# Performance work log

Hardware: AMD Instinct MI355X
Metric: run time of the kernel (lower is better)

Reference implementation:

```python
import jax, jax.numpy as jnp
import numpy as np

B, S, H = 2, 2048, 1024
NH = 16
HD = H // NH


def setup_inputs() -> dict:
    key = jax.random.key(0)
    ks = jax.random.split(key, 9)
    std = 1.0 / np.sqrt(H)
    inp = {"x": jax.random.normal(ks[0], (B, S, H), dtype=jnp.float32)}
    names = ["Wq", "Wk", "Wv", "Wo"]
    for i, n in enumerate(names):
        inp[n] = jax.random.uniform(ks[1 + i], (H, H), dtype=jnp.float32, minval=-std, maxval=std)
        inp["b" + n[1:]] = jax.random.uniform(ks[5 + i], (H,), dtype=jnp.float32, minval=-std, maxval=std)
    return inp


def reference(x, Wq, Wk, Wv, Wo, bq, bk, bv, bo):
    scale = HD ** -0.5
    # projections: torch Linear is x @ W.T + b
    def proj(W, b):
        y = jnp.einsum('bsh,oh->bso', x, W) + b
        return y.reshape(B, S, NH, HD).transpose(0, 2, 1, 3)  # [B, NH, S, HD]
    Q = proj(Wq, bq)
    K = proj(Wk, bk)
    V = proj(Wv, bv)
    scores = jnp.einsum('bhqd,bhkd->bhqk', Q, K) * scale  # [B, NH, S, S]
    attn = jax.nn.softmax(scores, axis=-1)
    ctx = jnp.einsum('bhqk,bhkd->bhqd', attn, V)
    ctx = ctx.transpose(0, 2, 1, 3).reshape(B, S, H)
    out = jnp.einsum('bsh,oh->bso', ctx, Wo) + bo
    avg_attention = attn.mean(axis=1).mean(axis=1)  # [B, S] (mean over heads, then query dim)
    return out, avg_attention
```

## Files before the change

kernel.cpp:

```cpp
#include <hip/hip_runtime.h>
#include <hip/hip_bf16.h>

#define B_  2
#define S_  2048
#define H_  1024
#define NH_ 16
#define HD_ 64
#define NTOK (B_*S_)

typedef __attribute__((ext_vector_type(8))) short bf16x8;
typedef __attribute__((ext_vector_type(4))) float f32x4;

#define SC2 0.18033688011112042f

static __device__ __forceinline__ ushort f2bf(float f) {
    __hip_bfloat16 h = __float2bfloat16(f);
    return *reinterpret_cast<ushort*>(&h);
}
static __device__ __forceinline__ uint cvt_pk_bf16(float lo, float hi) {
    uint r;
    asm("v_cvt_pk_bf16_f32 %0, %1, %2" : "=v"(r) : "v"(lo), "v"(hi));
    return r;
}

static __device__ __forceinline__ void gload_lds16(const void* g, void* l) {
    __builtin_amdgcn_global_load_lds(
        (const __attribute__((address_space(1))) void*)g,
        (__attribute__((address_space(3))) void*)l,
        16, 0, 0);
}

__global__ __launch_bounds__(256) void f32_to_bf16(
    const float* __restrict__ s, ushort* __restrict__ d, int n8)
{
    const int i = blockIdx.x * 256 + threadIdx.x;
    if (i >= n8) return;
    const float4 a = reinterpret_cast<const float4*>(s)[2*i + 0];
    const float4 b = reinterpret_cast<const float4*>(s)[2*i + 1];
    ushort u[8];
    u[0] = f2bf(a.x); u[1] = f2bf(a.y); u[2] = f2bf(a.z); u[3] = f2bf(a.w);
    u[4] = f2bf(b.x); u[5] = f2bf(b.y); u[6] = f2bf(b.z); u[7] = f2bf(b.w);
    reinterpret_cast<uint4*>(d)[i] = *reinterpret_cast<uint4*>(u);
}

struct Cvt4 { const float* s[4]; ushort* d[4]; };
__global__ __launch_bounds__(256) void w_to_bf16(Cvt4 a, int n8)
{
    const int z = blockIdx.y;
    const int i = blockIdx.x * 256 + threadIdx.x;
    if (i >= n8) return;
    const float* s = a.s[z];
    const float4 va = reinterpret_cast<const float4*>(s)[2*i + 0];
    const float4 vb = reinterpret_cast<const float4*>(s)[2*i + 1];
    ushort u[8];
    u[0] = f2bf(va.x); u[1] = f2bf(va.y); u[2] = f2bf(va.z); u[3] = f2bf(va.w);
    u[4] = f2bf(vb.x); u[5] = f2bf(vb.y); u[6] = f2bf(vb.z); u[7] = f2bf(vb.w);
    reinterpret_cast<uint4*>(a.d[z])[i] = *reinterpret_cast<uint4*>(u);
}

__global__ __launch_bounds__(256) void transpose_v(
    const ushort* __restrict__ Vb, ushort* __restrict__ Vt)
{
    __shared__ ushort T[64][72];
    const int t  = threadIdx.x;
    const int b  = blockIdx.z;
    const int h  = blockIdx.y;
    const int s0 = blockIdx.x * 64;
    const int r  = t >> 2;
    const int c0 = (t & 3) * 16;

    const ushort* src = Vb + (size_t)(b*S_ + s0 + r)*H_ + h*HD_ + c0;
    *reinterpret_cast<uint4*>(&T[r][c0])     = *reinterpret_cast<const uint4*>(src);
    *reinterpret_cast<uint4*>(&T[r][c0 + 8]) = *reinterpret_cast<const uint4*>(src + 8);
    __syncthreads();

    const int d = r;
    ushort tmp[16];
#pragma unroll
    for (int k = 0; k < 16; ++k) tmp[k] = T[c0 + k][d];
    ushort* dst = Vt + ((size_t)((b*NH_ + h)*HD_ + d))*S_ + s0 + c0;
    *reinterpret_cast<uint4*>(dst)     = *reinterpret_cast<uint4*>(&tmp[0]);
    *reinterpret_cast<uint4*>(dst + 8) = *reinterpret_cast<uint4*>(&tmp[8]);
}

struct GemmArgs {
    const ushort* W[3];
    const float*  bias[3];
    void*         Y[3];
    float         scale[3];
};

template<int MREP, bool BF16OUT>
__global__ __launch_bounds__(256) void gemm_mfma_bt(
    const ushort* __restrict__ A, GemmArgs args, int M, int N, int K)
{
    constexpr int BM = MREP * 32;
    __shared__ __align__(16) ushort As[BM * 64];
    __shared__ __align__(16) ushort Bs[128 * 64];

    const int z = blockIdx.z;
    const ushort* __restrict__ W   = args.W[z];
    const float*  __restrict__ bia = args.bias[z];
    const float sc = args.scale[z];

    const int t  = threadIdx.x;
    const int w  = t >> 6;
    const int l  = t & 63;
    const int lq = l >> 4;
    const int ln = l & 15;
    const int wr = w >> 1;
    const int wc = w & 1;
    const int m0 = blockIdx.x * BM;
    const int n0 = blockIdx.y * 128;
    const int srow = l >> 3;
    const int scol = (l & 7) * 8;

    f32x4 acc[MREP][4];
#pragma unroll
    for (int m = 0; m < MREP; ++m)
#pragma unroll
        for (int n = 0; n < 4; ++n) acc[m][n] = f32x4{0.f, 0.f, 0.f, 0.f};

    for (int k0 = 0; k0 < K; k0 += 64) {
        __syncthreads();
#pragma unroll
        for (int i = 0; i < BM/32; ++i) {
            const int rb = i*32 + w*8;
            gload_lds16(A + (size_t)(m0 + rb + srow)*K + k0 + scol, &As[rb*64]);
        }
#pragma unroll
        for (int i = 0; i < 4; ++i) {
            const int rb = i*32 + w*8;
            gload_lds16(W + (size_t)(n0 + rb + srow)*K + k0 + scol, &Bs[rb*64]);
        }
        __syncthreads();
#pragma unroll
        for (int ks = 0; ks < 2; ++ks) {
            bf16x8 bfr[4];
#pragma unroll
            for (int n = 0; n < 4; ++n)
                bfr[n] = *reinterpret_cast<const bf16x8*>(&Bs[(wc*64 + n*16 + ln)*64 + ks*32 + lq*8]);
#pragma unroll
            for (int m = 0; m < MREP; ++m) {
                const bf16x8 afr = *reinterpret_cast<const bf16x8*>(&As[(wr*MREP*16 + m*16 + ln)*64 + ks*32 + lq*8]);
#pragma unroll
                for (int n = 0; n < 4; ++n)
                    acc[m][n] = __builtin_amdgcn_mfma_f32_16x16x32_bf16(afr, bfr[n], acc[m][n], 0, 0, 0);
            }
        }
    }

    float bv[4];
#pragma unroll
    for (int n = 0; n < 4; ++n) bv[n] = bia[n0 + wc*64 + n*16 + ln];

#pragma unroll
    for (int m = 0; m < MREP; ++m) {
#pragma unroll
        for (int r = 0; r < 4; ++r) {
            const size_t row = (size_t)(m0 + wr*MREP*16 + m*16 + lq*4 + r);
#pragma unroll
            for (int n = 0; n < 4; ++n) {
                const int col = n0 + wc*64 + n*16 + ln;
                const float val = (acc[m][n][r] + bv[n]) * sc;
                if constexpr (BF16OUT)
                    ((ushort*)args.Y[z])[row*N + col] = f2bf(val);
                else
                    ((float*)args.Y[z])[row*N + col] = val;
            }
        }
    }
}

__global__ __launch_bounds__(256) void attn_pv(
    const ushort* __restrict__ Qb, const ushort* __restrict__ Kb,
    const ushort* __restrict__ Vtg, ushort* __restrict__ ctx,
    float* __restrict__ il2_g)
{
    __shared__ __align__(16) ushort Ks0[64*64];
    __shared__ __align__(16) ushort Ks1[64*64];
    __shared__ __align__(16) ushort Vs0[64*64];
    __shared__ __align__(16) ushort Vs1[64*64];
    __shared__ __align__(16) ushort Ps[4][16*64];

    const int t  = threadIdx.x;
    const int w  = t >> 6;
    const int l  = t & 63;
    const int lq = l >> 4;
    const int ln = l & 15;
    const int b  = blockIdx.z;
    const int h  = blockIdx.y;
    const int q0 = blockIdx.x * 64;
    const int ln7 = ln & 7;

    bf16x8 qf[2];
    {
        const ushort* qrow = Qb + ((size_t)(b*S_ + q0 + w*16 + ln))*H_ + h*HD_ + lq*8;
        qf[0] = *reinterpret_cast<const bf16x8*>(qrow);
        qf[1] = *reinterpret_cast<const bf16x8*>(qrow + 32);
    }

    bf16x8 onesb;
#pragma unroll
    for (int j = 0; j < 8; ++j) onesb[j] = (short)0x3F80;

    size_t koff[2], voff[2];
    int    dsto[2];
#pragma unroll
    for (int i = 0; i < 2; ++i) {
        const int chunk = i*256 + t;
        const int row   = chunk >> 3;
        const int c8    = (chunk & 7) ^ (row & 7);
        koff[i] = (size_t)(b*S_ + row)*H_ + h*HD_ + c8*8;
        voff[i] = ((size_t)((b*NH_ + h)*HD_ + row))*S_ + c8*8;
        dsto[i] = chunk*8;
    }

    f32x4 lsacc = f32x4{0.f, 0.f, 0.f, 0.f};
    f32x4 oacc[4];
#pragma unroll
    for (int nt = 0; nt < 4; ++nt) oacc[nt] = f32x4{0.f, 0.f, 0.f, 0.f};

    auto tile_body = [&](const ushort* __restrict__ ksb, const ushort* __restrict__ vsb,
                         int pre_kt, bool do_pre,
                         ushort* __restrict__ kdst, ushort* __restrict__ vdst) {
        if (do_pre) {
#pragma unroll
            for (int i = 0; i < 2; ++i) {
                gload_lds16(Kb + koff[i] + (size_t)pre_kt*H_, &kdst[dsto[i]]);
                gload_lds16(Vtg + voff[i] + pre_kt, &vdst[dsto[i]]);
            }
        }

        f32x4 sacc[4];
#pragma unroll
        for (int nt = 0; nt < 4; ++nt) sacc[nt] = f32x4{0.f, 0.f, 0.f, 0.f};
#pragma unroll
        for (int ks = 0; ks < 2; ++ks) {
            bf16x8 kb[4];
#pragma unroll
            for (int nt = 0; nt < 4; ++nt)
                kb[nt] = *reinterpret_cast<const bf16x8*>(
                    &ksb[(nt*16 + ln)*64 + (((ks*4 + lq) ^ ln7) * 8)]);
#pragma unroll
            for (int nt = 0; nt < 4; ++nt)
                sacc[nt] = __builtin_amdgcn_mfma_f32_16x16x32_bf16(
                    kb[nt], qf[ks], sacc[nt], 0, 0, 0);
        }

#pragma unroll
        for (int nt = 0; nt < 4; ++nt) {
            const float e0 = exp2f(sacc[nt][0]);
            const float e1 = exp2f(sacc[nt][1]);
            const float e2 = exp2f(sacc[nt][2]);
            const float e3 = exp2f(sacc[nt][3]);
            uint2 pk;
            pk.x = cvt_pk_bf16(e0, e1);
            pk.y = cvt_pk_bf16(e2, e3);
            const int wch = (nt*2 + (lq >> 1)) ^ ln7;
            *reinterpret_cast<uint2*>(&Ps[w][ln*64 + wch*8 + (lq & 1)*4]) = pk;
        }

#pragma unroll
        for (int ks = 0; ks < 2; ++ks) {
            const bf16x8 pa = *reinterpret_cast<const bf16x8*>(
                &Ps[w][ln*64 + (((ks*4 + lq) ^ ln7) * 8)]);
            lsacc = __builtin_amdgcn_mfma_f32_16x16x32_bf16(pa, onesb, lsacc, 0, 0, 0);
#pragma unroll
            for (int nt = 0; nt < 4; ++nt) {
                const bf16x8 vb8 = *reinterpret_cast<const bf16x8*>(
                    &vsb[(nt*16 + ln)*64 + (((ks*4 + lq) ^ ln7) * 8)]);
                oacc[nt] = __builtin_amdgcn_mfma_f32_16x16x32_bf16(
                    pa, vb8, oacc[nt], 0, 0, 0);
            }
        }

        __syncthreads();
    };

#pragma unroll
    for (int i = 0; i < 2; ++i) {
        gload_lds16(Kb + koff[i], &Ks0[dsto[i]]);
        gload_lds16(Vtg + voff[i], &Vs0[dsto[i]]);
    }
    __syncthreads();

    for (int kt = 0; kt < S_; kt += 128) {
        tile_body(Ks0, Vs0, kt + 64, true, Ks1, Vs1);
        tile_body(Ks1, Vs1, kt + 128, kt + 128 < S_, Ks0, Vs0);
    }

    float ivr[4];
#pragma unroll
    for (int r = 0; r < 4; ++r) ivr[r] = 1.f / lsacc[r];

    if (ln == 0) {
        float4 o;
        o.x = -__log2f(lsacc[0]);
        o.y = -__log2f(lsacc[1]);
        o.z = -__log2f(lsacc[2]);
        o.w = -__log2f(lsacc[3]);
        *reinterpret_cast<float4*>(
            il2_g + (size_t)(b*NH_ + h)*S_ + q0 + w*16 + lq*4) = o;
    }

    ushort* crow = ctx + ((size_t)(b*S_ + q0 + w*16 + lq*4))*H_ + h*HD_ + ln;
#pragma unroll
    for (int r = 0; r < 4; ++r)
#pragma unroll
        for (int nt = 0; nt < 4; ++nt)
            crow[(size_t)r*H_ + nt*16] = f2bf(oacc[nt][r] * ivr[r]);
}

__global__ __launch_bounds__(256) void attn_colsum(
    const ushort* __restrict__ Qb, const ushort* __restrict__ Kb,
    const float* __restrict__ il2_g, float* __restrict__ colsum)
{
    __shared__ __align__(16) ushort KsT[64*64];
    __shared__ __align__(16) ushort Qs0[64*64];
    __shared__ __align__(16) ushort Qs1[64*64];
    __shared__ __align__(16) float  iv[S_];

    const int t  = threadIdx.x;
    const int w  = t >> 6;
    const int l  = t & 63;
    const int lq = l >> 4;
    const int ln = l & 15;
    const int b  = blockIdx.z;
    const int h  = blockIdx.y;
    const int k0 = blockIdx.x * 64;
    const int bh = b*NH_ + h;
    const int ln7 = ln & 7;

    int crow_[2], cc8[2], dsto[2];
#pragma unroll
    for (int i = 0; i < 2; ++i) {
        const int chunk = i*256 + t;
        crow_[i] = chunk >> 3;
        cc8[i]   = (chunk & 7) ^ (crow_[i] & 7);
        dsto[i]  = chunk*8;
    }

#pragma unroll
    for (int i = 0; i < 2; ++i) {
        gload_lds16(Kb + (size_t)(b*S_ + k0 + crow_[i])*H_ + h*HD_ + cc8[i]*8, &KsT[dsto[i]]);
        gload_lds16(il2_g + (size_t)bh*S_ + (i*256 + t)*4, &iv[(i*256 + t)*4]);
        gload_lds16(Qb + (size_t)(b*S_ + crow_[i])*H_ + h*HD_ + cc8[i]*8, &Qs0[dsto[i]]);
    }
    __syncthreads();

    bf16x8 kf[2];
#pragma unroll
    for (int ks = 0; ks < 2; ++ks)
        kf[ks] = *reinterpret_cast<const bf16x8*>(
            &KsT[(w*16 + ln)*64 + (((ks*4 + lq) ^ ln7) * 8)]);

    float cs4[4] = {0.f, 0.f, 0.f, 0.f};

    auto tile_body = [&](const ushort* __restrict__ qsb,
                         int pre_qt, bool do_pre, ushort* __restrict__ qdst) {
        if (do_pre) {
#pragma unroll
            for (int i = 0; i < 2; ++i)
                gload_lds16(Qb + (size_t)(b*S_ + pre_qt + crow_[i])*H_ + h*HD_ + cc8[i]*8,
                            &qdst[dsto[i]]);
        }
#pragma unroll
        for (int c = 0; c < 4; ++c) {
            f32x4 sacc = f32x4{0.f, 0.f, 0.f, 0.f};
#pragma unroll
            for (int ks = 0; ks < 2; ++ks) {
                const bf16x8 af = *reinterpret_cast<const bf16x8*>(
                    &qsb[(c*16 + ln)*64 + (((ks*4 + lq) ^ ln7) * 8)]);
                sacc = __builtin_amdgcn_mfma_f32_16x16x32_bf16(af, kf[ks], sacc, 0, 0, 0);
            }
            const f32x4 iv4 = *reinterpret_cast<const f32x4*>(&iv[(c*16 + lq*4) + 0]);
            (void)iv4;
        }
        __syncthreads();
    };
    (void)tile_body;

    int qt = 0;
    for (; qt < S_; qt += 128) {
#pragma unroll
        for (int i = 0; i < 2; ++i)
            gload_lds16(Qb + (size_t)(b*S_ + qt + 64 + crow_[i])*H_ + h*HD_ + cc8[i]*8,
                        &Qs1[dsto[i]]);
#pragma unroll
        for (int c = 0; c < 4; ++c) {
            f32x4 sacc = f32x4{0.f, 0.f, 0.f, 0.f};
#pragma unroll
            for (int ks = 0; ks < 2; ++ks) {
                const bf16x8 af = *reinterpret_cast<const bf16x8*>(
                    &Qs0[(c*16 + ln)*64 + (((ks*4 + lq) ^ ln7) * 8)]);
                sacc = __builtin_amdgcn_mfma_f32_16x16x32_bf16(af, kf[ks], sacc, 0, 0, 0);
            }
            const f32x4 iv4 = *reinterpret_cast<const f32x4*>(&iv[qt + c*16 + lq*4]);
#pragma unroll
            for (int r = 0; r < 4; ++r)
                cs4[r] += exp2f(sacc[r] + iv4[r]);
        }
        __syncthreads();

        if (qt + 128 < S_) {
#pragma unroll
            for (int i = 0; i < 2; ++i)
                gload_lds16(Qb + (size_t)(b*S_ + qt + 128 + crow_[i])*H_ + h*HD_ + cc8[i]*8,
                            &Qs0[dsto[i]]);
        }
#pragma unroll
        for (int c = 0; c < 4; ++c) {
            f32x4 sacc = f32x4{0.f, 0.f, 0.f, 0.f};
#pragma unroll
            for (int ks = 0; ks < 2; ++ks) {
                const bf16x8 af = *reinterpret_cast<const bf16x8*>(
                    &Qs1[(c*16 + ln)*64 + (((ks*4 + lq) ^ ln7) * 8)]);
                sacc = __builtin_amdgcn_mfma_f32_16x16x32_bf16(af, kf[ks], sacc, 0, 0, 0);
            }
            const f32x4 iv4 = *reinterpret_cast<const f32x4*>(&iv[qt + 64 + c*16 + lq*4]);
#pragma unroll
            for (int r = 0; r < 4; ++r)
                cs4[r] += exp2f(sacc[r] + iv4[r]);
        }
        __syncthreads();
    }

    float cs = (cs4[0] + cs4[1]) + (cs4[2] + cs4[3]);
    cs += __shfl_xor(cs, 16);
    cs += __shfl_xor(cs, 32);
    if (l < 16)
        atomicAdd(&colsum[(size_t)b*S_ + k0 + w*16 + l], cs);
}

__global__ void zero_f32(float* p, int n)
{
    const int i = blockIdx.x * 256 + threadIdx.x;
    if (i < n) p[i] = 0.f;
}

__global__ void avg_write(const float* __restrict__ colsum, float* __restrict__ out, float inv)
{
    const int i = blockIdx.x * 256 + threadIdx.x;
    if (i < NTOK) out[i] = colsum[i] * inv;
}

extern "C" void kernel_launch(void* const* d_in, const int* in_sizes, int n_in,
                              void* d_out, int out_size, void* d_ws, size_t ws_size,
                              hipStream_t stream)
{
    const float* x  = (const float*)d_in[0];
    const float* Wq = (const float*)d_in[1];
    const float* bq = (const float*)d_in[2];
    const float* Wk = (const float*)d_in[3];
    const float* bk = (const float*)d_in[4];
    const float* Wv = (const float*)d_in[5];
    const float* bv = (const float*)d_in[6];
    const float* Wo = (const float*)d_in[7];
    const float* bo = (const float*)d_in[8];

    float* out     = (float*)d_out;
    float* avg_out = out + (size_t)NTOK * H_;

    char* ws = (char*)d_ws;
    const size_t mat  = (size_t)NTOK * H_ * sizeof(ushort);
    const size_t wmat = (size_t)H_ * H_ * sizeof(ushort);
    ushort* xb   = (ushort*)(ws);
    ushort* Qb   = (ushort*)(ws + mat);
    ushort* Kb   = (ushort*)(ws + 2*mat);
    ushort* Vb   = (ushort*)(ws + 3*mat);
    ushort* Vtg  = (ushort*)(ws + 4*mat);
    ushort* Wqb  = (ushort*)(ws + 5*mat);
    ushort* Wkb  = (ushort*)(ws + 5*mat + wmat);
    ushort* Wvb  = (ushort*)(ws + 5*mat + 2*wmat);
    ushort* Wob  = (ushort*)(ws + 5*mat + 3*wmat);
    float*  colsum = (float*)(ws + 5*mat + 4*wmat);
    float*  il2    = (float*)(ws + 5*mat + 4*wmat + 64*1024);
    ushort* ctxb = xb;

    const dim3 blk(256);

    f32_to_bf16<<<dim3((NTOK*H_/8 + 255)/256), blk, 0, stream>>>(x, xb, NTOK*H_/8);
    {
        Cvt4 c;
        c.s[0] = Wq; c.s[1] = Wk; c.s[2] = Wv; c.s[3] = Wo;
        c.d[0] = Wqb; c.d[1] = Wkb; c.d[2] = Wvb; c.d[3] = Wob;
        w_to_bf16<<<dim3((H_*H_/8 + 255)/256, 4), blk, 0, stream>>>(c, H_*H_/8);
    }

    zero_f32<<<dim3((NTOK + 255)/256), blk, 0, stream>>>(colsum, NTOK);

    {
        GemmArgs ga;
        ga.W[0] = Wqb; ga.W[1] = Wkb; ga.W[2] = Wvb;
        ga.bias[0] = bq; ga.bias[1] = bk; ga.bias[2] = bv;
        ga.Y[0] = Qb; ga.Y[1] = Kb; ga.Y[2] = Vb;
        ga.scale[0] = SC2; ga.scale[1] = 1.f; ga.scale[2] = 1.f;
        gemm_mfma_bt<4, true><<<dim3(NTOK/128, H_/128, 3), blk, 0, stream>>>(
            xb, ga, NTOK, H_, H_);
    }

    transpose_v<<<dim3(S_/64, NH_, B_), blk, 0, stream>>>(Vb, Vtg);

    attn_pv<<<dim3(S_/64, NH_, B_), blk, 0, stream>>>(Qb, Kb, Vtg, ctxb, il2);
    attn_colsum<<<dim3(S_/64, NH_, B_), blk, 0, stream>>>(Qb, Kb, il2, colsum);

    {
        GemmArgs ga;
        ga.W[0] = Wob; ga.W[1] = Wob; ga.W[2] = Wob;
        ga.bias[0] = bo; ga.bias[1] = bo; ga.bias[2] = bo;
        ga.Y[0] = out; ga.Y[1] = out; ga.Y[2] = out;
        ga.scale[0] = 1.f; ga.scale[1] = 1.f; ga.scale[2] = 1.f;
        gemm_mfma_bt<2, false><<<dim3(NTOK/64, H_/128, 1), blk, 0, stream>>>(
            ctxb, ga, NTOK, H_, H_);
    }

    avg_write<<<dim3((NTOK + 255)/256), blk, 0, stream>>>(colsum, avg_out, 1.f/((float)NH_ * (float)S_));
}
```

Measured before the change: 203.0 us.

## Merge prep kernels and run colsum concurrently with output projection in one launch

```diff
diff --git a/kernel.cpp b/kernel.cpp
--- a/kernel.cpp
+++ b/kernel.cpp
@@ -30,11 +30,15 @@
         16, 0, 0);
 }
 
-__global__ __launch_bounds__(256) void f32_to_bf16(
-    const float* __restrict__ s, ushort* __restrict__ d, int n8)
-{
-    const int i = blockIdx.x * 256 + threadIdx.x;
-    if (i >= n8) return;
+struct PrepArgs {
+    const float* src[5];
+    ushort*      dst[5];
+    float*       zero;
+};
+
+static __device__ __forceinline__ void conv8(const float* __restrict__ s,
+                                             ushort* __restrict__ d, int i)
+{
     const float4 a = reinterpret_cast<const float4*>(s)[2*i + 0];
     const float4 b = reinterpret_cast<const float4*>(s)[2*i + 1];
     ushort u[8];
@@ -43,19 +47,24 @@
     reinterpret_cast<uint4*>(d)[i] = *reinterpret_cast<uint4*>(u);
 }
 
-struct Cvt4 { const float* s[4]; ushort* d[4]; };
-__global__ __launch_bounds__(256) void w_to_bf16(Cvt4 a, int n8)
-{
-    const int z = blockIdx.y;
-    const int i = blockIdx.x * 256 + threadIdx.x;
-    if (i >= n8) return;
-    const float* s = a.s[z];
-    const float4 va = reinterpret_cast<const float4*>(s)[2*i + 0];
-    const float4 vb = reinterpret_cast<const float4*>(s)[2*i + 1];
-    ushort u[8];
-    u[0] = f2bf(va.x); u[1] = f2bf(va.y); u[2] = f2bf(va.z); u[3] = f2bf(va.w);
-    u[4] = f2bf(vb.x); u[5] = f2bf(vb.y); u[6] = f2bf(vb.z); u[7] = f2bf(vb.w);
-    reinterpret_cast<uint4*>(a.d[z])[i] = *reinterpret_cast<uint4*>(u);
+__global__ __launch_bounds__(256) void prep(PrepArgs a)
+{
+    int bid = blockIdx.x;
+    const int t = threadIdx.x;
+    if (bid < 2048) {
+        conv8(a.src[0], a.dst[0], bid*256 + t);
+        return;
+    }
+    bid -= 2048;
+    if (bid < 2048) {
+        const int wi = 1 + (bid >> 9);
+        const int i  = (bid & 511)*256 + t;
+        conv8(a.src[wi], a.dst[wi], i);
+        return;
+    }
+    bid -= 2048;
+    const int i = bid*256 + t;
+    if (i < NTOK) a.zero[i] = 0.f;
 }
 
 __global__ __launch_bounds__(256) void transpose_v(
@@ -90,10 +99,10 @@
     float         scale[3];
 };
 
-template<int MREP, bool BF16OUT>
-__global__ __launch_bounds__(256) void gemm_mfma_bt(
+__global__ __launch_bounds__(256) void gemm_qkv(
     const ushort* __restrict__ A, GemmArgs args, int M, int N, int K)
 {
+    constexpr int MREP = 4;
     constexpr int BM = MREP * 32;
     __shared__ __align__(16) ushort As[BM * 64];
     __shared__ __align__(16) ushort Bs[128 * 64];
@@ -154,6 +163,7 @@
 #pragma unroll
     for (int n = 0; n < 4; ++n) bv[n] = bia[n0 + wc*64 + n*16 + ln];
 
+    ushort* Y = (ushort*)args.Y[z];
 #pragma unroll
     for (int m = 0; m < MREP; ++m) {
 #pragma unroll
@@ -162,11 +172,7 @@
 #pragma unroll
             for (int n = 0; n < 4; ++n) {
                 const int col = n0 + wc*64 + n*16 + ln;
-                const float val = (acc[m][n][r] + bv[n]) * sc;
-                if constexpr (BF16OUT)
-                    ((ushort*)args.Y[z])[row*N + col] = f2bf(val);
-                else
-                    ((float*)args.Y[z])[row*N + col] = val;
+                Y[row*N + col] = f2bf((acc[m][n][r] + bv[n]) * sc);
             }
         }
     }
@@ -312,131 +318,173 @@
             crow[(size_t)r*H_ + nt*16] = f2bf(oacc[nt][r] * ivr[r]);
 }
 
-__global__ __launch_bounds__(256) void attn_colsum(
-    const ushort* __restrict__ Qb, const ushort* __restrict__ Kb,
-    const float* __restrict__ il2_g, float* __restrict__ colsum)
-{
-    __shared__ __align__(16) ushort KsT[64*64];
-    __shared__ __align__(16) ushort Qs0[64*64];
-    __shared__ __align__(16) ushort Qs1[64*64];
-    __shared__ __align__(16) float  iv[S_];
-
+struct FusedArgs {
+    const ushort* Qb; const ushort* Kb;
+    const float*  il2; float* colsum;
+    const ushort* A;  const ushort* W;
+    const float*  bias; float* Y;
+};
+
+__global__ __launch_bounds__(256) void colsum_outproj(FusedArgs fa)
+{
+    __shared__ __align__(16) char smem[32768];
+    const int id = blockIdx.x;
     const int t  = threadIdx.x;
     const int w  = t >> 6;
     const int l  = t & 63;
     const int lq = l >> 4;
     const int ln = l & 15;
-    const int b  = blockIdx.z;
-    const int h  = blockIdx.y;
-    const int k0 = blockIdx.x * 64;
-    const int bh = b*NH_ + h;
     const int ln7 = ln & 7;
 
-    int crow_[2], cc8[2], dsto[2];
-#pragma unroll
-    for (int i = 0; i < 2; ++i) {
-        const int chunk = i*256 + t;
-        crow_[i] = chunk >> 3;
-        cc8[i]   = (chunk & 7) ^ (crow_[i] & 7);
-        dsto[i]  = chunk*8;
-    }
-
-#pragma unroll
-    for (int i = 0; i < 2; ++i) {
-        gload_lds16(Kb + (size_t)(b*S_ + k0 + crow_[i])*H_ + h*HD_ + cc8[i]*8, &KsT[dsto[i]]);
-        gload_lds16(il2_g + (size_t)bh*S_ + (i*256 + t)*4, &iv[(i*256 + t)*4]);
-        gload_lds16(Qb + (size_t)(b*S_ + crow_[i])*H_ + h*HD_ + cc8[i]*8, &Qs0[dsto[i]]);
-    }
-    __syncthreads();
-
-    bf16x8 kf[2];
-#pragma unroll
-    for (int ks = 0; ks < 2; ++ks)
-        kf[ks] = *reinterpret_cast<const bf16x8*>(
-            &KsT[(w*16 + ln)*64 + (((ks*4 + lq) ^ ln7) * 8)]);
-
-    float cs4[4] = {0.f, 0.f, 0.f, 0.f};
-
-    auto tile_body = [&](const ushort* __restrict__ qsb,
-                         int pre_qt, bool do_pre, ushort* __restrict__ qdst) {
-        if (do_pre) {
+    if (id < 1024) {
+        ushort* KsT = (ushort*)smem;
+        ushort* Qs0 = (ushort*)(smem + 8192);
+        ushort* Qs1 = (ushort*)(smem + 16384);
+        float*  iv  = (float*)(smem + 24576);
+
+        const int k0 = (id & 31) * 64;
+        const int h  = (id >> 5) & 15;
+        const int b  = id >> 9;
+        const int bh = b*NH_ + h;
+
+        int crow_[2], cc8[2], dsto[2];
+#pragma unroll
+        for (int i = 0; i < 2; ++i) {
+            const int chunk = i*256 + t;
+            crow_[i] = chunk >> 3;
+            cc8[i]   = (chunk & 7) ^ (crow_[i] & 7);
+            dsto[i]  = chunk*8;
+        }
+
+#pragma unroll
+        for (int i = 0; i < 2; ++i) {
+            gload_lds16(fa.Kb + (size_t)(b*S_ + k0 + crow_[i])*H_ + h*HD_ + cc8[i]*8, &KsT[dsto[i]]);
+            gload_lds16(fa.il2 + (size_t)bh*S_ + (i*256 + t)*4, &iv[(i*256 + t)*4]);
+            gload_lds16(fa.Qb + (size_t)(b*S_ + crow_[i])*H_ + h*HD_ + cc8[i]*8, &Qs0[dsto[i]]);
+        }
+        __syncthreads();
+
+        bf16x8 kf[2];
+#pragma unroll
+        for (int ks = 0; ks < 2; ++ks)
+            kf[ks] = *reinterpret_cast<const bf16x8*>(
+                &KsT[(w*16 + ln)*64 + (((ks*4 + lq) ^ ln7) * 8)]);
+
+        float cs4[4] = {0.f, 0.f, 0.f, 0.f};
+
+        for (int qt = 0; qt < S_; qt += 128) {
 #pragma unroll
             for (int i = 0; i < 2; ++i)
-                gload_lds16(Qb + (size_t)(b*S_ + pre_qt + crow_[i])*H_ + h*HD_ + cc8[i]*8,
-                            &qdst[dsto[i]]);
-        }
-#pragma unroll
-        for (int c = 0; c < 4; ++c) {
-            f32x4 sacc = f32x4{0.f, 0.f, 0.f, 0.f};
+                gload_lds16(fa.Qb + (size_t)(b*S_ + qt + 64 + crow_[i])*H_ + h*HD_ + cc8[i]*8,
+                            &Qs1[dsto[i]]);
+#pragma unroll
+            for (int c = 0; c < 4; ++c) {
+                f32x4 sacc = f32x4{0.f, 0.f, 0.f, 0.f};
+#pragma unroll
+                for (int ks = 0; ks < 2; ++ks) {
+                    const bf16x8 af = *reinterpret_cast<const bf16x8*>(
+                        &Qs0[(c*16 + ln)*64 + (((ks*4 + lq) ^ ln7) * 8)]);
+                    sacc = __builtin_amdgcn_mfma_f32_16x16x32_bf16(af, kf[ks], sacc, 0, 0, 0);
+                }
+                const f32x4 iv4 = *reinterpret_cast<const f32x4*>(&iv[qt + c*16 + lq*4]);
+#pragma unroll
+                for (int r = 0; r < 4; ++r)
+                    cs4[r] += exp2f(sacc[r] + iv4[r]);
+            }
+            __syncthreads();
+
+            if (qt + 128 < S_) {
+#pragma unroll
+                for (int i = 0; i < 2; ++i)
+                    gload_lds16(fa.Qb + (size_t)(b*S_ + qt + 128 + crow_[i])*H_ + h*HD_ + cc8[i]*8,
+                                &Qs0[dsto[i]]);
+            }
+#pragma unroll
+            for (int c = 0; c < 4; ++c) {
+                f32x4 sacc = f32x4{0.f, 0.f, 0.f, 0.f};
+#pragma unroll
+                for (int ks = 0; ks < 2; ++ks) {
+                    const bf16x8 af = *reinterpret_cast<const bf16x8*>(
+                        &Qs1[(c*16 + ln)*64 + (((ks*4 + lq) ^ ln7) * 8)]);
+                    sacc = __builtin_amdgcn_mfma_f32_16x16x32_bf16(af, kf[ks], sacc, 0, 0, 0);
+                }
+                const f32x4 iv4 = *reinterpret_cast<const f32x4*>(&iv[qt + 64 + c*16 + lq*4]);
+#pragma unroll
+                for (int r = 0; r < 4; ++r)
+                    cs4[r] += exp2f(sacc[r] + iv4[r]);
+            }
+            __syncthreads();
+        }
+
+        float cs = (cs4[0] + cs4[1]) + (cs4[2] + cs4[3]);
+        cs += __shfl_xor(cs, 16);
+        cs += __shfl_xor(cs, 32);
+        if (l < 16)
+            atomicAdd(&fa.colsum[(size_t)b*S_ + k0 + w*16 + l], cs);
+    } else {
+        ushort* As = (ushort*)smem;
+        ushort* Bs = (ushort*)(smem + 8192);
+
+        const int g  = id - 1024;
+        const int m0 = (g & 63) * 64;
+        const int n0 = (g >> 6) * 128;
+        const int wr = w >> 1;
+        const int wc = w & 1;
+        const int srow = l >> 3;
+        const int scol = (l & 7) * 8;
+
+        f32x4 acc[2][4];
+#pragma unroll
+        for (int m = 0; m < 2; ++m)
+#pragma unroll
+            for (int n = 0; n < 4; ++n) acc[m][n] = f32x4{0.f, 0.f, 0.f, 0.f};
+
+        for (int k0 = 0; k0 < H_; k0 += 64) {
+            __syncthreads();
+#pragma unroll
+            for (int i = 0; i < 2; ++i) {
+                const int rb = i*32 + w*8;
+                gload_lds16(fa.A + (size_t)(m0 + rb + srow)*H_ + k0 + scol, &As[rb*64]);
+            }
+#pragma unroll
+            for (int i = 0; i < 4; ++i) {
+                const int rb = i*32 + w*8;
+                gload_lds16(fa.W + (size_t)(n0 + rb + srow)*H_ + k0 + scol, &Bs[rb*64]);
+            }
+            __syncthreads();
 #pragma unroll
             for (int ks = 0; ks < 2; ++ks) {
-                const bf16x8 af = *reinterpret_cast<const bf16x8*>(
-                    &qsb[(c*16 + ln)*64 + (((ks*4 + lq) ^ ln7) * 8)]);
-                sacc = __builtin_amdgcn_mfma_f32_16x16x32_bf16(af, kf[ks], sacc, 0, 0, 0);
-            }
-            const f32x4 iv4 = *reinterpret_cast<const f32x4*>(&iv[(c*16 + lq*4) + 0]);
-            (void)iv4;
-        }
-        __syncthreads();
-    };
-    (void)tile_body;
-
-    int qt = 0;
-    for (; qt < S_; qt += 128) {
-#pragma unroll
-        for (int i = 0; i < 2; ++i)
-            gload_lds16(Qb + (size_t)(b*S_ + qt + 64 + crow_[i])*H_ + h*HD_ + cc8[i]*8,
-                        &Qs1[dsto[i]]);
-#pragma unroll
-        for (int c = 0; c < 4; ++c) {
-            f32x4 sacc = f32x4{0.f, 0.f, 0.f, 0.f};
-#pragma unroll
-            for (int ks = 0; ks < 2; ++ks) {
-                const bf16x8 af = *reinterpret_cast<const bf16x8*>(
-                    &Qs0[(c*16 + ln)*64 + (((ks*4 + lq) ^ ln7) * 8)]);
-                sacc = __builtin_amdgcn_mfma_f32_16x16x32_bf16(af, kf[ks], sacc, 0, 0, 0);
-            }
-            const f32x4 iv4 = *reinterpret_cast<const f32x4*>(&iv[qt + c*16 + lq*4]);
-#pragma unroll
-            for (int r = 0; r < 4; ++r)
-                cs4[r] += exp2f(sacc[r] + iv4[r]);
-        }
-        __syncthreads();
-
-        if (qt + 128 < S_) {
-#pragma unroll
-            for (int i = 0; i < 2; ++i)
-                gload_lds16(Qb + (size_t)(b*S_ + qt + 128 + crow_[i])*H_ + h*HD_ + cc8[i]*8,
-                            &Qs0[dsto[i]]);
-        }
-#pragma unroll
-        for (int c = 0; c < 4; ++c) {
-            f32x4 sacc = f32x4{0.f, 0.f, 0.f, 0.f};
-#pragma unroll
-            for (int ks = 0; ks < 2; ++ks) {
-                const bf16x8 af = *reinterpret_cast<const bf16x8*>(
-                    &Qs1[(c*16 + ln)*64 + (((ks*4 + lq) ^ ln7) * 8)]);
-                sacc = __builtin_amdgcn_mfma_f32_16x16x32_bf16(af, kf[ks], sacc, 0, 0, 0);
-            }
-            const f32x4 iv4 = *reinterpret_cast<const f32x4*>(&iv[qt + 64 + c*16 + lq*4]);
-#pragma unroll
-            for (int r = 0; r < 4; ++r)
-                cs4[r] += exp2f(sacc[r] + iv4[r]);
-        }
-        __syncthreads();
-    }
-
-    float cs = (cs4[0] + cs4[1]) + (cs4[2] + cs4[3]);
-    cs += __shfl_xor(cs, 16);
-    cs += __shfl_xor(cs, 32);
-    if (l < 16)
-        atomicAdd(&colsum[(size_t)b*S_ + k0 + w*16 + l], cs);
-}
-
-__global__ void zero_f32(float* p, int n)
-{
-    const int i = blockIdx.x * 256 + threadIdx.x;
-    if (i < n) p[i] = 0.f;
+                bf16x8 bfr[4];
+#pragma unroll
+                for (int n = 0; n < 4; ++n)
+                    bfr[n] = *reinterpret_cast<const bf16x8*>(&Bs[(wc*64 + n*16 + ln)*64 + ks*32 + lq*8]);
+#pragma unroll
+                for (int m = 0; m < 2; ++m) {
+                    const bf16x8 afr = *reinterpret_cast<const bf16x8*>(&As[(wr*32 + m*16 + ln)*64 + ks*32 + lq*8]);
+#pragma unroll
+                    for (int n = 0; n < 4; ++n)
+                        acc[m][n] = __builtin_amdgcn_mfma_f32_16x16x32_bf16(afr, bfr[n], acc[m][n], 0, 0, 0);
+                }
+            }
+        }
+
+        float bv[4];
+#pragma unroll
+        for (int n = 0; n < 4; ++n) bv[n] = fa.bias[n0 + wc*64 + n*16 + ln];
+
+#pragma unroll
+        for (int m = 0; m < 2; ++m) {
+#pragma unroll
+            for (int r = 0; r < 4; ++r) {
+                const size_t row = (size_t)(m0 + wr*32 + m*16 + lq*4 + r);
+#pragma unroll
+                for (int n = 0; n < 4; ++n) {
+                    const int col = n0 + wc*64 + n*16 + ln;
+                    fa.Y[row*H_ + col] = acc[m][n][r] + bv[n];
+                }
+            }
+        }
+    }
 }
 
 __global__ void avg_write(const float* __restrict__ colsum, float* __restrict__ out, float inv)
@@ -480,15 +528,16 @@
 
     const dim3 blk(256);
 
-    f32_to_bf16<<<dim3((NTOK*H_/8 + 255)/256), blk, 0, stream>>>(x, xb, NTOK*H_/8);
     {
-        Cvt4 c;
-        c.s[0] = Wq; c.s[1] = Wk; c.s[2] = Wv; c.s[3] = Wo;
-        c.d[0] = Wqb; c.d[1] = Wkb; c.d[2] = Wvb; c.d[3] = Wob;
-        w_to_bf16<<<dim3((H_*H_/8 + 255)/256, 4), blk, 0, stream>>>(c, H_*H_/8);
-    }
-
-    zero_f32<<<dim3((NTOK + 255)/256), blk, 0, stream>>>(colsum, NTOK);
+        PrepArgs pa;
+        pa.src[0] = x;  pa.dst[0] = xb;
+        pa.src[1] = Wq; pa.dst[1] = Wqb;
+        pa.src[2] = Wk; pa.dst[2] = Wkb;
+        pa.src[3] = Wv; pa.dst[3] = Wvb;
+        pa.src[4] = Wo; pa.dst[4] = Wob;
+        pa.zero = colsum;
+        prep<<<dim3(4112), blk, 0, stream>>>(pa);
+    }
 
     {
         GemmArgs ga;
@@ -496,23 +545,18 @@
         ga.bias[0] = bq; ga.bias[1] = bk; ga.bias[2] = bv;
         ga.Y[0] = Qb; ga.Y[1] = Kb; ga.Y[2] = Vb;
         ga.scale[0] = SC2; ga.scale[1] = 1.f; ga.scale[2] = 1.f;
-        gemm_mfma_bt<4, true><<<dim3(NTOK/128, H_/128, 3), blk, 0, stream>>>(
-            xb, ga, NTOK, H_, H_);
+        gemm_qkv<<<dim3(NTOK/128, H_/128, 3), blk, 0, stream>>>(xb, ga, NTOK, H_, H_);
     }
 
     transpose_v<<<dim3(S_/64, NH_, B_), blk, 0, stream>>>(Vb, Vtg);
 
     attn_pv<<<dim3(S_/64, NH_, B_), blk, 0, stream>>>(Qb, Kb, Vtg, ctxb, il2);
-    attn_colsum<<<dim3(S_/64, NH_, B_), blk, 0, stream>>>(Qb, Kb, il2, colsum);
 
     {
-        GemmArgs ga;
-        ga.W[0] = Wob; ga.W[1] = Wob; ga.W[2] = Wob;
-        ga.bias[0] = bo; ga.bias[1] = bo; ga.bias[2] = bo;
-        ga.Y[0] = out; ga.Y[1] = out; ga.Y[2] = out;
-        ga.scale[0] = 1.f; ga.scale[1] = 1.f; ga.scale[2] = 1.f;
-        gemm_mfma_bt<2, false><<<dim3(NTOK/64, H_/128, 1), blk, 0, stream>>>(
-            ctxb, ga, NTOK, H_, H_);
+        FusedArgs fa;
+        fa.Qb = Qb; fa.Kb = Kb; fa.il2 = il2; fa.colsum = colsum;
+        fa.A = ctxb; fa.W = Wob; fa.bias = bo; fa.Y = out;
+        colsum_outproj<<<dim3(1536), blk, 0, stream>>>(fa);
     }
 
     avg_write<<<dim3((NTOK + 255)/256), blk, 0, stream>>>(colsum, avg_out, 1.f/((float)NH_ * (float)S_));
```

Measured after the change: 183.0 us. 1.11x faster.
